# Kernel optimization log

Hardware: AMD Instinct MI355X
Metric: run time of the kernel (lower is better)

The kernel has to match this reference:

```python
import jax, jax.numpy as jnp
import numpy as np

D = 4096   # ray_hidden_dim / embed_dim
H = 2      # num_heads
E = 8192   # expert hidden dim
OUT = 1    # out_dim


def setup_inputs() -> dict:
    key = jax.random.key(0)
    ks = jax.random.split(key, 18)
    def w(k, shape, fan_in):
        return jax.random.normal(k, shape, jnp.float32) * (1.0 / np.sqrt(fan_in))
    return dict(
        ray=jax.random.uniform(ks[0], (2,), jnp.float32),
        emb1_w=w(ks[1], (D, 1), 1), emb1_b=w(ks[2], (D,), 1),
        emb2_w=w(ks[3], (D, 1), 1), emb2_b=w(ks[4], (D,), 1),
        attn_in_w=w(ks[5], (3 * D, D), D), attn_in_b=jnp.zeros((3 * D,), jnp.float32),
        attn_out_w=w(ks[6], (D, D), D), attn_out_b=jnp.zeros((D,), jnp.float32),
        ffn1_w=w(ks[7], (D, D), D), ffn1_b=w(ks[8], (D,), D),
        ffn2_w=w(ks[9], (D, D), D), ffn2_b=w(ks[10], (D,), D),
        exp_w1=w(ks[11], (E, D), D), exp_b1=w(ks[12], (E,), D),
        exp_w2=w(ks[13], (OUT, E), E), exp_b2=w(ks[14], (OUT,), E),
        idx=0,
    )


def reference(ray, emb1_w, emb1_b, emb2_w, emb2_b,
              attn_in_w, attn_in_b, attn_out_w, attn_out_b,
              ffn1_w, ffn1_b, ffn2_w, ffn2_b,
              exp_w1, exp_b1, exp_w2, exp_b2, idx):
    # per-task embeddings: Linear(1, D) + ReLU on each scalar ray component
    e1 = jax.nn.relu(ray[0:1] @ emb1_w.T + emb1_b)  # [D]
    e2 = jax.nn.relu(ray[1:2] @ emb2_w.T + emb2_b)  # [D]
    x = jnp.stack([e1, e2])                          # [L=2, D] (batch=1 squeezed)

    # multi-head self-attention (torch MHA, packed in_proj)
    qkv = x @ attn_in_w.T + attn_in_b                # [2, 3D]
    q, k, v = jnp.split(qkv, 3, axis=-1)
    hd = D // H
    q = q.reshape(2, H, hd) * jnp.float32(1.0 / np.sqrt(hd))
    k = k.reshape(2, H, hd)
    v = v.reshape(2, H, hd)
    scores = jnp.einsum('lhd,mhd->hlm', q, k)        # [H, 2, 2]
    attn = jax.nn.softmax(scores, axis=-1)
    o = jnp.einsum('hlm,mhd->lhd', attn, v).reshape(2, D)
    x = x + (o @ attn_out_w.T + attn_out_b)          # residual 1

    # FFN block with residual
    x = x + (jax.nn.relu(x @ ffn1_w.T + ffn1_b) @ ffn2_w.T + ffn2_b)

    # expert MLP (idx selects expert; n_experts=1 so idx==0) then mean over seq
    y = jax.nn.relu(x @ exp_w1.T + exp_b1) @ exp_w2.T + exp_b2  # [2, OUT]
    return jnp.mean(y, axis=0)                       # [OUT]
```

## Files before the change

kernel.cpp:

```cpp
#include <hip/hip_runtime.h>

#define D4 4096
#define E8 8192

#define OFF_X    0
#define OFF_QKV  8192
#define OFF_O    32768
#define OFF_H    40960
#define OFF_G    49152
__device__ float g_ws[65536];

__global__ void k_embed(const float* __restrict__ ray,
                        const float* __restrict__ w1,
                        const float* __restrict__ b1,
                        const float* __restrict__ w2,
                        const float* __restrict__ b2) {
    int i = blockIdx.x * blockDim.x + threadIdx.x;
    if (i < D4) {
        float r0 = ray[0], r1 = ray[1];
        g_ws[OFF_X + i]      = fmaxf(fmaf(r0, w1[i], b1[i]), 0.f);
        g_ws[OFF_X + D4 + i] = fmaxf(fmaf(r1, w2[i], b2[i]), 0.f);
    }
}

__global__ __launch_bounds__(512, 4) void k_gemv2(
        const float* __restrict__ W,
        const float* __restrict__ bias,
        int xin_off, int out_off, int resid_off,
        int R, int relu_flag) {
    __shared__ float sx[2 * D4];
    const float* xin = g_ws + xin_off;
    int tid = threadIdx.x;
    #pragma unroll
    for (int it = 0; it < (2 * D4) / (512 * 4); ++it) {
        int j = (it * 512 + tid) * 4;
        *(float4*)(sx + j) = *(const float4*)(xin + j);
    }
    __syncthreads();

    int row  = blockIdx.x * 8 + (tid >> 6);
    int lane = tid & 63;
    const float* wrow = W + (size_t)row * D4;
    float acc0 = 0.f, acc1 = 0.f;
    #pragma unroll 4
    for (int it = 0; it < D4 / (64 * 4); ++it) {
        int j = (it * 64 + lane) * 4;
        float4 wv = *(const float4*)(wrow + j);
        float4 x0 = *(const float4*)(sx + j);
        float4 x1 = *(const float4*)(sx + D4 + j);
        acc0 = fmaf(wv.x, x0.x, fmaf(wv.y, x0.y, fmaf(wv.z, x0.z, fmaf(wv.w, x0.w, acc0))));
        acc1 = fmaf(wv.x, x1.x, fmaf(wv.y, x1.y, fmaf(wv.z, x1.z, fmaf(wv.w, x1.w, acc1))));
    }
    #pragma unroll
    for (int off = 32; off; off >>= 1) {
        acc0 += __shfl_down(acc0, off);
        acc1 += __shfl_down(acc1, off);
    }
    if (lane == 0) {
        float b  = bias[row];
        float r0 = acc0 + b, r1 = acc1 + b;
        if (resid_off >= 0) {
            r0 += g_ws[resid_off + row];
            r1 += g_ws[resid_off + R + row];
        }
        if (relu_flag) { r0 = fmaxf(r0, 0.f); r1 = fmaxf(r1, 0.f); }
        g_ws[out_off + row]     = r0;
        g_ws[out_off + R + row] = r1;
    }
}

__global__ void k_attn() {
    const int HD = D4 / 2;
    const float* qkv = g_ws + OFF_QKV;
    float* o = g_ws + OFF_O;
    __shared__ float sred[8][16];
    __shared__ float sattn[2][2][2];
    int tid = threadIdx.x, lane = tid & 63, wave = tid >> 6;

    float a000 = 0.f, a001 = 0.f, a010 = 0.f, a011 = 0.f;
    float a100 = 0.f, a101 = 0.f, a110 = 0.f, a111 = 0.f;
    #pragma unroll
    for (int it = 0; it < 2; ++it) {
        int i = it * 1024 + tid;
        float q0 = qkv[0 * 3 * D4 + i];
        float q1 = qkv[1 * 3 * D4 + i];
        float k0 = qkv[0 * 3 * D4 + D4 + i];
        float k1 = qkv[1 * 3 * D4 + D4 + i];
        a000 += q0 * k0; a001 += q0 * k1;
        a010 += q1 * k0; a011 += q1 * k1;
    }
    #pragma unroll
    for (int it = 0; it < 2; ++it) {
        int i = HD + it * 1024 + tid;
        float q0 = qkv[0 * 3 * D4 + i];
        float q1 = qkv[1 * 3 * D4 + i];
        float k0 = qkv[0 * 3 * D4 + D4 + i];
        float k1 = qkv[1 * 3 * D4 + D4 + i];
        a100 += q0 * k0; a101 += q0 * k1;
        a110 += q1 * k0; a111 += q1 * k1;
    }
    #define WREDUCE(v, idx) { float t_ = (v); \
        _Pragma("unroll") \
        for (int off_ = 32; off_; off_ >>= 1) t_ += __shfl_down(t_, off_); \
        if (lane == 0) sred[idx][wave] = t_; }
    WREDUCE(a000, 0) WREDUCE(a001, 1) WREDUCE(a010, 2) WREDUCE(a011, 3)
    WREDUCE(a100, 4) WREDUCE(a101, 5) WREDUCE(a110, 6) WREDUCE(a111, 7)
    #undef WREDUCE
    __syncthreads();
    if (tid == 0) {
        float scale = rsqrtf((float)HD);
        for (int h = 0; h < 2; h++)
            for (int l = 0; l < 2; l++) {
                float s0 = 0.f, s1 = 0.f;
                for (int w = 0; w < 16; w++) {
                    s0 += sred[(h * 2 + l) * 2 + 0][w];
                    s1 += sred[(h * 2 + l) * 2 + 1][w];
                }
                s0 *= scale; s1 *= scale;
                float mx = fmaxf(s0, s1);
                float e0 = __expf(s0 - mx), e1 = __expf(s1 - mx);
                float inv = 1.f / (e0 + e1);
                sattn[h][l][0] = e0 * inv;
                sattn[h][l][1] = e1 * inv;
            }
    }
    __syncthreads();
    #pragma unroll
    for (int it = 0; it < 4; ++it) {
        int i = it * 1024 + tid;
        int h = i >> 11;
        float v0 = qkv[0 * 3 * D4 + 2 * D4 + i];
        float v1 = qkv[1 * 3 * D4 + 2 * D4 + i];
        o[i]      = sattn[h][0][0] * v0 + sattn[h][0][1] * v1;
        o[D4 + i] = sattn[h][1][0] * v0 + sattn[h][1][1] * v1;
    }
}

__global__ void k_expert_out(const float* __restrict__ w2,
                             const float* __restrict__ b2,
                             float* __restrict__ out) {
    const float* g = g_ws + OFF_G;
    __shared__ float sred[2][16];
    int tid = threadIdx.x, lane = tid & 63, wave = tid >> 6;
    float a0 = 0.f, a1 = 0.f;
    #pragma unroll
    for (int it = 0; it < E8 / 1024; ++it) {
        int e = it * 1024 + tid;
        float w = w2[e];
        a0 += w * g[e];
        a1 += w * g[E8 + e];
    }
    #pragma unroll
    for (int off = 32; off; off >>= 1) {
        a0 += __shfl_down(a0, off);
        a1 += __shfl_down(a1, off);
    }
    if (lane == 0) { sred[0][wave] = a0; sred[1][wave] = a1; }
    __syncthreads();
    if (tid == 0) {
        float b = b2[0];
        float y0 = b, y1 = b;
        for (int w = 0; w < 16; w++) { y0 += sred[0][w]; y1 += sred[1][w]; }
        out[0] = 0.5f * (y0 + y1);
    }
}

extern "C" void kernel_launch(void* const* d_in, const int* in_sizes, int n_in,
                              void* d_out, int out_size, void* d_ws, size_t ws_size,
                              hipStream_t stream) {
    const float* ray        = (const float*)d_in[0];
    const float* emb1_w     = (const float*)d_in[1];
    const float* emb1_b     = (const float*)d_in[2];
    const float* emb2_w     = (const float*)d_in[3];
    const float* emb2_b     = (const float*)d_in[4];
    const float* attn_in_w  = (const float*)d_in[5];
    const float* attn_in_b  = (const float*)d_in[6];
    const float* attn_out_w = (const float*)d_in[7];
    const float* attn_out_b = (const float*)d_in[8];
    const float* ffn1_w     = (const float*)d_in[9];
    const float* ffn1_b     = (const float*)d_in[10];
    const float* ffn2_w     = (const float*)d_in[11];
    const float* ffn2_b     = (const float*)d_in[12];
    const float* exp_w1     = (const float*)d_in[13];
    const float* exp_b1     = (const float*)d_in[14];
    const float* exp_w2     = (const float*)d_in[15];
    const float* exp_b2     = (const float*)d_in[16];
    float* out = (float*)d_out;
    (void)d_ws; (void)ws_size; (void)in_sizes; (void)n_in;

    k_embed<<<(D4 + 255) / 256, 256, 0, stream>>>(ray, emb1_w, emb1_b, emb2_w, emb2_b);
    k_gemv2<<<3 * D4 / 8, 512, 0, stream>>>(attn_in_w, attn_in_b, OFF_X, OFF_QKV, -1, 3 * D4, 0);
    k_attn<<<1, 1024, 0, stream>>>();
    k_gemv2<<<D4 / 8, 512, 0, stream>>>(attn_out_w, attn_out_b, OFF_O, OFF_X, OFF_X, D4, 0);
    k_gemv2<<<D4 / 8, 512, 0, stream>>>(ffn1_w, ffn1_b, OFF_X, OFF_H, -1, D4, 1);
    k_gemv2<<<D4 / 8, 512, 0, stream>>>(ffn2_w, ffn2_b, OFF_H, OFF_X, OFF_X, D4, 0);
    k_gemv2<<<E8 / 8, 512, 0, stream>>>(exp_w1, exp_b1, OFF_X, OFF_G, -1, E8, 1);
    k_expert_out<<<1, 1024, 0, stream>>>(exp_w2, exp_b2, out);
}
```

Before: 509.1 us.

## Restructure GEMV to one float4 per thread with two rows per block

Replaces the shared-memory-staged GEMV, where each wave loops over a full row, with a kernel that assigns two rows to a 1024-thread block. Each thread loads a single float4 from each row and reads the activation vector directly from global memory, then reduces across waves via shared memory. The aim is to raise memory-level parallelism and remove the per-block staging of x. The trade-off is many more small blocks plus an extra block-level sync and reduction per pair of rows.

```diff
diff --git a/kernel.cpp b/kernel.cpp
--- a/kernel.cpp
+++ b/kernel.cpp
@@ -23,49 +23,65 @@
     }
 }
 
-__global__ __launch_bounds__(512, 4) void k_gemv2(
+__global__ __launch_bounds__(1024) void k_gemv_row(
         const float* __restrict__ W,
         const float* __restrict__ bias,
         int xin_off, int out_off, int resid_off,
         int R, int relu_flag) {
-    __shared__ float sx[2 * D4];
+    int tid  = threadIdx.x;
+    int r0   = blockIdx.x * 2;
+    int j    = tid * 4;
     const float* xin = g_ws + xin_off;
-    int tid = threadIdx.x;
-    #pragma unroll
-    for (int it = 0; it < (2 * D4) / (512 * 4); ++it) {
-        int j = (it * 512 + tid) * 4;
-        *(float4*)(sx + j) = *(const float4*)(xin + j);
-    }
-    __syncthreads();
-
-    int row  = blockIdx.x * 8 + (tid >> 6);
-    int lane = tid & 63;
-    const float* wrow = W + (size_t)row * D4;
-    float acc0 = 0.f, acc1 = 0.f;
-    #pragma unroll 4
-    for (int it = 0; it < D4 / (64 * 4); ++it) {
-        int j = (it * 64 + lane) * 4;
-        float4 wv = *(const float4*)(wrow + j);
-        float4 x0 = *(const float4*)(sx + j);
-        float4 x1 = *(const float4*)(sx + D4 + j);
-        acc0 = fmaf(wv.x, x0.x, fmaf(wv.y, x0.y, fmaf(wv.z, x0.z, fmaf(wv.w, x0.w, acc0))));
-        acc1 = fmaf(wv.x, x1.x, fmaf(wv.y, x1.y, fmaf(wv.z, x1.z, fmaf(wv.w, x1.w, acc1))));
-    }
+    const float* w0p = W + (size_t)r0 * D4 + j;
+
+    float4 w0 = *(const float4*)(w0p);
+    float4 w1 = *(const float4*)(w0p + D4);
+    float4 x0 = *(const float4*)(xin + j);
+    float4 x1 = *(const float4*)(xin + D4 + j);
+
+    float a00 = w0.x*x0.x + w0.y*x0.y + w0.z*x0.z + w0.w*x0.w;
+    float a01 = w0.x*x1.x + w0.y*x1.y + w0.z*x1.z + w0.w*x1.w;
+    float a10 = w1.x*x0.x + w1.y*x0.y + w1.z*x0.z + w1.w*x0.w;
+    float a11 = w1.x*x1.x + w1.y*x1.y + w1.z*x1.z + w1.w*x1.w;
+
     #pragma unroll
     for (int off = 32; off; off >>= 1) {
-        acc0 += __shfl_down(acc0, off);
-        acc1 += __shfl_down(acc1, off);
-    }
+        a00 += __shfl_down(a00, off);
+        a01 += __shfl_down(a01, off);
+        a10 += __shfl_down(a10, off);
+        a11 += __shfl_down(a11, off);
+    }
+    __shared__ float sred[16][4];
+    int lane = tid & 63, wave = tid >> 6;
     if (lane == 0) {
-        float b  = bias[row];
-        float r0 = acc0 + b, r1 = acc1 + b;
+        sred[wave][0] = a00; sred[wave][1] = a01;
+        sred[wave][2] = a10; sred[wave][3] = a11;
+    }
+    __syncthreads();
+    if (tid == 0) {
+        float s00 = 0.f, s01 = 0.f, s10 = 0.f, s11 = 0.f;
+        #pragma unroll
+        for (int w = 0; w < 16; ++w) {
+            s00 += sred[w][0]; s01 += sred[w][1];
+            s10 += sred[w][2]; s11 += sred[w][3];
+        }
+        int r1i = r0 + 1;
+        float b0 = bias[r0], b1 = bias[r1i];
+        s00 += b0; s01 += b0; s10 += b1; s11 += b1;
         if (resid_off >= 0) {
-            r0 += g_ws[resid_off + row];
-            r1 += g_ws[resid_off + R + row];
+            s00 += g_ws[resid_off + r0];
+            s01 += g_ws[resid_off + R + r0];
+            s10 += g_ws[resid_off + r1i];
+            s11 += g_ws[resid_off + R + r1i];
         }
-        if (relu_flag) { r0 = fmaxf(r0, 0.f); r1 = fmaxf(r1, 0.f); }
-        g_ws[out_off + row]     = r0;
-        g_ws[out_off + R + row] = r1;
+        if (relu_flag) {
+            s00 = fmaxf(s00, 0.f); s01 = fmaxf(s01, 0.f);
+            s10 = fmaxf(s10, 0.f); s11 = fmaxf(s11, 0.f);
+        }
+        g_ws[out_off + r0]       = s00;
+        g_ws[out_off + R + r0]   = s01;
+        g_ws[out_off + r1i]      = s10;
+        g_ws[out_off + R + r1i]  = s11;
     }
 }
 
@@ -189,11 +205,11 @@
     (void)d_ws; (void)ws_size; (void)in_sizes; (void)n_in;
 
     k_embed<<<(D4 + 255) / 256, 256, 0, stream>>>(ray, emb1_w, emb1_b, emb2_w, emb2_b);
-    k_gemv2<<<3 * D4 / 8, 512, 0, stream>>>(attn_in_w, attn_in_b, OFF_X, OFF_QKV, -1, 3 * D4, 0);
+    k_gemv_row<<<3 * D4 / 2, 1024, 0, stream>>>(attn_in_w, attn_in_b, OFF_X, OFF_QKV, -1, 3 * D4, 0);
     k_attn<<<1, 1024, 0, stream>>>();
-    k_gemv2<<<D4 / 8, 512, 0, stream>>>(attn_out_w, attn_out_b, OFF_O, OFF_X, OFF_X, D4, 0);
-    k_gemv2<<<D4 / 8, 512, 0, stream>>>(ffn1_w, ffn1_b, OFF_X, OFF_H, -1, D4, 1);
-    k_gemv2<<<D4 / 8, 512, 0, stream>>>(ffn2_w, ffn2_b, OFF_H, OFF_X, OFF_X, D4, 0);
-    k_gemv2<<<E8 / 8, 512, 0, stream>>>(exp_w1, exp_b1, OFF_X, OFF_G, -1, E8, 1);
+    k_gemv_row<<<D4 / 2, 1024, 0, stream>>>(attn_out_w, attn_out_b, OFF_O, OFF_X, OFF_X, D4, 0);
+    k_gemv_row<<<D4 / 2, 1024, 0, stream>>>(ffn1_w, ffn1_b, OFF_X, OFF_H, -1, D4, 1);
+    k_gemv_row<<<D4 / 2, 1024, 0, stream>>>(ffn2_w, ffn2_b, OFF_H, OFF_X, OFF_X, D4, 0);
+    k_gemv_row<<<E8 / 2, 1024, 0, stream>>>(exp_w1, exp_b1, OFF_X, OFF_G, -1, E8, 1);
     k_expert_out<<<1, 1024, 0, stream>>>(exp_w2, exp_b2, out);
 }
```

New measurement: 512.6 us. About the same (+0.7%).

## Fuse whole forward pass into one persistent cooperative kernel with grid syncs

Applied to the files above, without the earlier changes.

Replaces eight separate launches (embed, five GEMVs, attention, expert output) with a single cooperative kernel of 256 blocks by 1024 threads that runs every stage and separates them with grid.sync. Embeddings are computed straight into shared memory, and the attention mix writes its output into shared memory so the next GEMV reads it without a global round trip. The GEMV loop now loads eight float4 weight values per batch before doing the math, to keep more memory requests in flight. The aim is to remove launch gaps and inter-kernel drain. In exchange, each block of 16 waves shares one block's resources and relies on grid-wide barriers, and the attention-score stage keeps only 8 blocks busy while the rest wait.

```diff
diff --git a/kernel.cpp b/kernel.cpp
--- a/kernel.cpp
+++ b/kernel.cpp
@@ -1,199 +1,209 @@
 #include <hip/hip_runtime.h>
+#include <hip/hip_cooperative_groups.h>
+
+namespace cg = cooperative_groups;
 
 #define D4 4096
 #define E8 8192
+#define NBLK 256
+#define NTHR 1024
+#define NWAVES (NBLK * (NTHR / 64))
 
 #define OFF_X    0
 #define OFF_QKV  8192
-#define OFF_O    32768
+#define OFF_XO   32768
 #define OFF_H    40960
-#define OFF_G    49152
-__device__ float g_ws[65536];
-
-__global__ void k_embed(const float* __restrict__ ray,
-                        const float* __restrict__ w1,
-                        const float* __restrict__ b1,
-                        const float* __restrict__ w2,
-                        const float* __restrict__ b2) {
-    int i = blockIdx.x * blockDim.x + threadIdx.x;
-    if (i < D4) {
-        float r0 = ray[0], r1 = ray[1];
-        g_ws[OFF_X + i]      = fmaxf(fmaf(r0, w1[i], b1[i]), 0.f);
-        g_ws[OFF_X + D4 + i] = fmaxf(fmaf(r1, w2[i], b2[i]), 0.f);
+#define OFF_X2   49152
+#define OFF_G    57344
+#define OFF_S    73728
+__device__ float g_ws[73744];
+
+struct P {
+    const float *ray, *e1w, *e1b, *e2w, *e2b;
+    const float *aiw, *aib, *aow, *aob;
+    const float *f1w, *f1b, *f2w, *f2b;
+    const float *xw1, *xb1, *xw2, *xb2;
+    float *out;
+};
+
+__device__ __forceinline__ void gemv2_lds(
+        const float* __restrict__ W, const float* __restrict__ bias,
+        const float* sx, float* out, const float* resid,
+        int R, int relu, int lane, int gwave)
+{
+    for (int r = gwave; r < R; r += NWAVES) {
+        const float* wrow = W + (size_t)r * D4;
+        float a0 = 0.f, a1 = 0.f;
+        #pragma unroll
+        for (int c = 0; c < 2; ++c) {
+            float4 wv[8];
+            #pragma unroll
+            for (int k = 0; k < 8; ++k)
+                wv[k] = *(const float4*)(wrow + ((c * 8 + k) * 64 + lane) * 4);
+            #pragma unroll
+            for (int k = 0; k < 8; ++k) {
+                int j = ((c * 8 + k) * 64 + lane) * 4;
+                float4 x0 = *(const float4*)(sx + j);
+                float4 x1 = *(const float4*)(sx + D4 + j);
+                a0 += wv[k].x*x0.x + wv[k].y*x0.y + wv[k].z*x0.z + wv[k].w*x0.w;
+                a1 += wv[k].x*x1.x + wv[k].y*x1.y + wv[k].z*x1.z + wv[k].w*x1.w;
+            }
+        }
+        #pragma unroll
+        for (int off = 32; off; off >>= 1) {
+            a0 += __shfl_down(a0, off);
+            a1 += __shfl_down(a1, off);
+        }
+        if (lane == 0) {
+            float b = bias[r];
+            float r0 = a0 + b, r1 = a1 + b;
+            if (resid) { r0 += resid[r]; r1 += resid[R + r]; }
+            if (relu)  { r0 = fmaxf(r0, 0.f); r1 = fmaxf(r1, 0.f); }
+            out[r] = r0; out[R + r] = r1;
+        }
     }
 }
 
-__global__ __launch_bounds__(512, 4) void k_gemv2(
-        const float* __restrict__ W,
-        const float* __restrict__ bias,
-        int xin_off, int out_off, int resid_off,
-        int R, int relu_flag) {
+__global__ __launch_bounds__(NTHR) void k_fused(P p) {
+    cg::grid_group grid = cg::this_grid();
     __shared__ float sx[2 * D4];
-    const float* xin = g_ws + xin_off;
-    int tid = threadIdx.x;
-    #pragma unroll
-    for (int it = 0; it < (2 * D4) / (512 * 4); ++it) {
-        int j = (it * 512 + tid) * 4;
-        *(float4*)(sx + j) = *(const float4*)(xin + j);
-    }
-    __syncthreads();
-
-    int row  = blockIdx.x * 8 + (tid >> 6);
-    int lane = tid & 63;
-    const float* wrow = W + (size_t)row * D4;
-    float acc0 = 0.f, acc1 = 0.f;
-    #pragma unroll 4
-    for (int it = 0; it < D4 / (64 * 4); ++it) {
-        int j = (it * 64 + lane) * 4;
-        float4 wv = *(const float4*)(wrow + j);
-        float4 x0 = *(const float4*)(sx + j);
-        float4 x1 = *(const float4*)(sx + D4 + j);
-        acc0 = fmaf(wv.x, x0.x, fmaf(wv.y, x0.y, fmaf(wv.z, x0.z, fmaf(wv.w, x0.w, acc0))));
-        acc1 = fmaf(wv.x, x1.x, fmaf(wv.y, x1.y, fmaf(wv.z, x1.z, fmaf(wv.w, x1.w, acc1))));
-    }
-    #pragma unroll
-    for (int off = 32; off; off >>= 1) {
-        acc0 += __shfl_down(acc0, off);
-        acc1 += __shfl_down(acc1, off);
-    }
-    if (lane == 0) {
-        float b  = bias[row];
-        float r0 = acc0 + b, r1 = acc1 + b;
-        if (resid_off >= 0) {
-            r0 += g_ws[resid_off + row];
-            r1 += g_ws[resid_off + R + row];
-        }
-        if (relu_flag) { r0 = fmaxf(r0, 0.f); r1 = fmaxf(r1, 0.f); }
-        g_ws[out_off + row]     = r0;
-        g_ws[out_off + R + row] = r1;
-    }
-}
-
-__global__ void k_attn() {
-    const int HD = D4 / 2;
-    const float* qkv = g_ws + OFF_QKV;
-    float* o = g_ws + OFF_O;
-    __shared__ float sred[8][16];
-    __shared__ float sattn[2][2][2];
+    __shared__ float sred[16];
+    __shared__ float sred2[16][2];
     int tid = threadIdx.x, lane = tid & 63, wave = tid >> 6;
-
-    float a000 = 0.f, a001 = 0.f, a010 = 0.f, a011 = 0.f;
-    float a100 = 0.f, a101 = 0.f, a110 = 0.f, a111 = 0.f;
-    #pragma unroll
-    for (int it = 0; it < 2; ++it) {
-        int i = it * 1024 + tid;
-        float q0 = qkv[0 * 3 * D4 + i];
-        float q1 = qkv[1 * 3 * D4 + i];
-        float k0 = qkv[0 * 3 * D4 + D4 + i];
-        float k1 = qkv[1 * 3 * D4 + D4 + i];
-        a000 += q0 * k0; a001 += q0 * k1;
-        a010 += q1 * k0; a011 += q1 * k1;
-    }
-    #pragma unroll
-    for (int it = 0; it < 2; ++it) {
-        int i = HD + it * 1024 + tid;
-        float q0 = qkv[0 * 3 * D4 + i];
-        float q1 = qkv[1 * 3 * D4 + i];
-        float k0 = qkv[0 * 3 * D4 + D4 + i];
-        float k1 = qkv[1 * 3 * D4 + D4 + i];
-        a100 += q0 * k0; a101 += q0 * k1;
-        a110 += q1 * k0; a111 += q1 * k1;
-    }
-    #define WREDUCE(v, idx) { float t_ = (v); \
-        _Pragma("unroll") \
-        for (int off_ = 32; off_; off_ >>= 1) t_ += __shfl_down(t_, off_); \
-        if (lane == 0) sred[idx][wave] = t_; }
-    WREDUCE(a000, 0) WREDUCE(a001, 1) WREDUCE(a010, 2) WREDUCE(a011, 3)
-    WREDUCE(a100, 4) WREDUCE(a101, 5) WREDUCE(a110, 6) WREDUCE(a111, 7)
-    #undef WREDUCE
-    __syncthreads();
-    if (tid == 0) {
-        float scale = rsqrtf((float)HD);
-        for (int h = 0; h < 2; h++)
-            for (int l = 0; l < 2; l++) {
-                float s0 = 0.f, s1 = 0.f;
-                for (int w = 0; w < 16; w++) {
-                    s0 += sred[(h * 2 + l) * 2 + 0][w];
-                    s1 += sred[(h * 2 + l) * 2 + 1][w];
-                }
-                s0 *= scale; s1 *= scale;
+    int gwave = blockIdx.x * (NTHR / 64) + wave;
+
+    float r0 = p.ray[0], r1 = p.ray[1];
+    #pragma unroll
+    for (int it = 0; it < 4; ++it) {
+        int i = it * NTHR + tid;
+        sx[i]      = fmaxf(fmaf(r0, p.e1w[i], p.e1b[i]), 0.f);
+        sx[D4 + i] = fmaxf(fmaf(r1, p.e2w[i], p.e2b[i]), 0.f);
+    }
+    __syncthreads();
+    if (blockIdx.x == 0) {
+        #pragma unroll
+        for (int it = 0; it < 8; ++it) {
+            int i = it * NTHR + tid;
+            g_ws[OFF_X + i] = sx[i];
+        }
+    }
+    gemv2_lds(p.aiw, p.aib, sx, g_ws + OFF_QKV, nullptr, 3 * D4, 0, lane, gwave);
+    grid.sync();
+
+    if (blockIdx.x < 8) {
+        int b = blockIdx.x;
+        int h = b >> 2, l = (b >> 1) & 1, m = b & 1;
+        const float* q = g_ws + OFF_QKV + l * 3 * D4 + h * 2048;
+        const float* k = g_ws + OFF_QKV + m * 3 * D4 + D4 + h * 2048;
+        float acc = q[tid * 2] * k[tid * 2] + q[tid * 2 + 1] * k[tid * 2 + 1];
+        #pragma unroll
+        for (int off = 32; off; off >>= 1) acc += __shfl_down(acc, off);
+        if (lane == 0) sred[wave] = acc;
+        __syncthreads();
+        if (tid == 0) {
+            float s = 0.f;
+            for (int w = 0; w < 16; ++w) s += sred[w];
+            g_ws[OFF_S + b] = s;
+        }
+    }
+    grid.sync();
+
+    {
+        float scale = rsqrtf(2048.f);
+        float pr[2][2][2];
+        #pragma unroll
+        for (int h = 0; h < 2; ++h)
+            #pragma unroll
+            for (int l = 0; l < 2; ++l) {
+                float s0 = g_ws[OFF_S + h * 4 + l * 2 + 0] * scale;
+                float s1 = g_ws[OFF_S + h * 4 + l * 2 + 1] * scale;
                 float mx = fmaxf(s0, s1);
                 float e0 = __expf(s0 - mx), e1 = __expf(s1 - mx);
                 float inv = 1.f / (e0 + e1);
-                sattn[h][l][0] = e0 * inv;
-                sattn[h][l][1] = e1 * inv;
+                pr[h][l][0] = e0 * inv; pr[h][l][1] = e1 * inv;
             }
-    }
-    __syncthreads();
-    #pragma unroll
-    for (int it = 0; it < 4; ++it) {
-        int i = it * 1024 + tid;
-        int h = i >> 11;
-        float v0 = qkv[0 * 3 * D4 + 2 * D4 + i];
-        float v1 = qkv[1 * 3 * D4 + 2 * D4 + i];
-        o[i]      = sattn[h][0][0] * v0 + sattn[h][0][1] * v1;
-        o[D4 + i] = sattn[h][1][0] * v0 + sattn[h][1][1] * v1;
-    }
-}
-
-__global__ void k_expert_out(const float* __restrict__ w2,
-                             const float* __restrict__ b2,
-                             float* __restrict__ out) {
-    const float* g = g_ws + OFF_G;
-    __shared__ float sred[2][16];
-    int tid = threadIdx.x, lane = tid & 63, wave = tid >> 6;
-    float a0 = 0.f, a1 = 0.f;
-    #pragma unroll
-    for (int it = 0; it < E8 / 1024; ++it) {
-        int e = it * 1024 + tid;
-        float w = w2[e];
-        a0 += w * g[e];
-        a1 += w * g[E8 + e];
-    }
-    #pragma unroll
-    for (int off = 32; off; off >>= 1) {
-        a0 += __shfl_down(a0, off);
-        a1 += __shfl_down(a1, off);
-    }
-    if (lane == 0) { sred[0][wave] = a0; sred[1][wave] = a1; }
-    __syncthreads();
-    if (tid == 0) {
-        float b = b2[0];
-        float y0 = b, y1 = b;
-        for (int w = 0; w < 16; w++) { y0 += sred[0][w]; y1 += sred[1][w]; }
-        out[0] = 0.5f * (y0 + y1);
+        #pragma unroll
+        for (int it = 0; it < 4; ++it) {
+            int i = it * NTHR + tid;
+            const int h = it >> 1;
+            float v0 = g_ws[OFF_QKV + 0 * 3 * D4 + 2 * D4 + i];
+            float v1 = g_ws[OFF_QKV + 1 * 3 * D4 + 2 * D4 + i];
+            sx[i]      = pr[h][0][0] * v0 + pr[h][0][1] * v1;
+            sx[D4 + i] = pr[h][1][0] * v0 + pr[h][1][1] * v1;
+        }
+        __syncthreads();
+        gemv2_lds(p.aow, p.aob, sx, g_ws + OFF_XO, g_ws + OFF_X, D4, 0, lane, gwave);
+    }
+    grid.sync();
+
+    #pragma unroll
+    for (int it = 0; it < 2; ++it) {
+        int j = (it * NTHR + tid) * 4;
+        *(float4*)(sx + j) = *(const float4*)(g_ws + OFF_XO + j);
+    }
+    __syncthreads();
+    gemv2_lds(p.f1w, p.f1b, sx, g_ws + OFF_H, nullptr, D4, 1, lane, gwave);
+    grid.sync();
+
+    #pragma unroll
+    for (int it = 0; it < 2; ++it) {
+        int j = (it * NTHR + tid) * 4;
+        *(float4*)(sx + j) = *(const float4*)(g_ws + OFF_H + j);
+    }
+    __syncthreads();
+    gemv2_lds(p.f2w, p.f2b, sx, g_ws + OFF_X2, g_ws + OFF_XO, D4, 0, lane, gwave);
+    grid.sync();
+
+    #pragma unroll
+    for (int it = 0; it < 2; ++it) {
+        int j = (it * NTHR + tid) * 4;
+        *(float4*)(sx + j) = *(const float4*)(g_ws + OFF_X2 + j);
+    }
+    __syncthreads();
+    gemv2_lds(p.xw1, p.xb1, sx, g_ws + OFF_G, nullptr, E8, 1, lane, gwave);
+    grid.sync();
+
+    if (blockIdx.x == 0) {
+        float a0 = 0.f, a1 = 0.f;
+        #pragma unroll
+        for (int it = 0; it < 8; ++it) {
+            int e = it * NTHR + tid;
+            float w = p.xw2[e];
+            a0 += w * g_ws[OFF_G + e];
+            a1 += w * g_ws[OFF_G + E8 + e];
+        }
+        #pragma unroll
+        for (int off = 32; off; off >>= 1) {
+            a0 += __shfl_down(a0, off);
+            a1 += __shfl_down(a1, off);
+        }
+        if (lane == 0) { sred2[wave][0] = a0; sred2[wave][1] = a1; }
+        __syncthreads();
+        if (tid == 0) {
+            float y0 = 0.f, y1 = 0.f;
+            for (int w = 0; w < 16; ++w) { y0 += sred2[w][0]; y1 += sred2[w][1]; }
+            p.out[0] = 0.5f * (y0 + y1) + p.xb2[0];
+        }
     }
 }
 
 extern "C" void kernel_launch(void* const* d_in, const int* in_sizes, int n_in,
                               void* d_out, int out_size, void* d_ws, size_t ws_size,
                               hipStream_t stream) {
-    const float* ray        = (const float*)d_in[0];
-    const float* emb1_w     = (const float*)d_in[1];
-    const float* emb1_b     = (const float*)d_in[2];
-    const float* emb2_w     = (const float*)d_in[3];
-    const float* emb2_b     = (const float*)d_in[4];
-    const float* attn_in_w  = (const float*)d_in[5];
-    const float* attn_in_b  = (const float*)d_in[6];
-    const float* attn_out_w = (const float*)d_in[7];
-    const float* attn_out_b = (const float*)d_in[8];
-    const float* ffn1_w     = (const float*)d_in[9];
-    const float* ffn1_b     = (const float*)d_in[10];
-    const float* ffn2_w     = (const float*)d_in[11];
-    const float* ffn2_b     = (const float*)d_in[12];
-    const float* exp_w1     = (const float*)d_in[13];
-    const float* exp_b1     = (const float*)d_in[14];
-    const float* exp_w2     = (const float*)d_in[15];
-    const float* exp_b2     = (const float*)d_in[16];
-    float* out = (float*)d_out;
     (void)d_ws; (void)ws_size; (void)in_sizes; (void)n_in;
-
-    k_embed<<<(D4 + 255) / 256, 256, 0, stream>>>(ray, emb1_w, emb1_b, emb2_w, emb2_b);
-    k_gemv2<<<3 * D4 / 8, 512, 0, stream>>>(attn_in_w, attn_in_b, OFF_X, OFF_QKV, -1, 3 * D4, 0);
-    k_attn<<<1, 1024, 0, stream>>>();
-    k_gemv2<<<D4 / 8, 512, 0, stream>>>(attn_out_w, attn_out_b, OFF_O, OFF_X, OFF_X, D4, 0);
-    k_gemv2<<<D4 / 8, 512, 0, stream>>>(ffn1_w, ffn1_b, OFF_X, OFF_H, -1, D4, 1);
-    k_gemv2<<<D4 / 8, 512, 0, stream>>>(ffn2_w, ffn2_b, OFF_H, OFF_X, OFF_X, D4, 0);
-    k_gemv2<<<E8 / 8, 512, 0, stream>>>(exp_w1, exp_b1, OFF_X, OFF_G, -1, E8, 1);
-    k_expert_out<<<1, 1024, 0, stream>>>(exp_w2, exp_b2, out);
+    P p;
+    p.ray = (const float*)d_in[0];
+    p.e1w = (const float*)d_in[1];  p.e1b = (const float*)d_in[2];
+    p.e2w = (const float*)d_in[3];  p.e2b = (const float*)d_in[4];
+    p.aiw = (const float*)d_in[5];  p.aib = (const float*)d_in[6];
+    p.aow = (const float*)d_in[7];  p.aob = (const float*)d_in[8];
+    p.f1w = (const float*)d_in[9];  p.f1b = (const float*)d_in[10];
+    p.f2w = (const float*)d_in[11]; p.f2b = (const float*)d_in[12];
+    p.xw1 = (const float*)d_in[13]; p.xb1 = (const float*)d_in[14];
+    p.xw2 = (const float*)d_in[15]; p.xb2 = (const float*)d_in[16];
+    p.out = (float*)d_out;
+
+    void* args[] = { &p };
+    hipLaunchCooperativeKernel((void*)k_fused, dim3(NBLK), dim3(NTHR),
+                               args, 0u, stream);
 }
```

Result: slower. 846.3 us (+66.2%).

## Split GEMV rows across two waves and preload weights into registers

Applied to the files above, without the earlier changes.

Replaces the LDS-staged GEMV with a kernel where each pair of waves covers one weight row, each wave taking half of it. All eight float4 weight loads are issued up front into registers, and the activations are read straight from global memory instead of being copied into LDS. The two half-row results are combined through a small shared buffer. The aim is more loads in flight and no 32KB LDS fill plus barrier per block, so the weight stream runs closer to memory bandwidth. The cost is more blocks, a cross-wave reduction, and activation re-reads that depend on L2 hits.

```diff
diff --git a/kernel.cpp b/kernel.cpp
--- a/kernel.cpp
+++ b/kernel.cpp
@@ -23,49 +23,46 @@
     }
 }
 
-__global__ __launch_bounds__(512, 4) void k_gemv2(
+__global__ __launch_bounds__(256, 8) void k_gemv_h(
         const float* __restrict__ W,
         const float* __restrict__ bias,
         int xin_off, int out_off, int resid_off,
         int R, int relu_flag) {
-    __shared__ float sx[2 * D4];
-    const float* xin = g_ws + xin_off;
-    int tid = threadIdx.x;
+    int tid = threadIdx.x, lane = tid & 63, wave = tid >> 6;
+    int r  = blockIdx.x * 2 + (wave >> 1);
+    int hf = wave & 1;
+    const float* wp = W + (size_t)r * D4 + hf * 2048;
+    const float* xp = g_ws + xin_off + hf * 2048;
+
+    float4 wv[8];
     #pragma unroll
-    for (int it = 0; it < (2 * D4) / (512 * 4); ++it) {
-        int j = (it * 512 + tid) * 4;
-        *(float4*)(sx + j) = *(const float4*)(xin + j);
-    }
-    __syncthreads();
+    for (int k = 0; k < 8; ++k)
+        wv[k] = *(const float4*)(wp + (k * 64 + lane) * 4);
 
-    int row  = blockIdx.x * 8 + (tid >> 6);
-    int lane = tid & 63;
-    const float* wrow = W + (size_t)row * D4;
-    float acc0 = 0.f, acc1 = 0.f;
-    #pragma unroll 4
-    for (int it = 0; it < D4 / (64 * 4); ++it) {
-        int j = (it * 64 + lane) * 4;
-        float4 wv = *(const float4*)(wrow + j);
-        float4 x0 = *(const float4*)(sx + j);
-        float4 x1 = *(const float4*)(sx + D4 + j);
-        acc0 = fmaf(wv.x, x0.x, fmaf(wv.y, x0.y, fmaf(wv.z, x0.z, fmaf(wv.w, x0.w, acc0))));
-        acc1 = fmaf(wv.x, x1.x, fmaf(wv.y, x1.y, fmaf(wv.z, x1.z, fmaf(wv.w, x1.w, acc1))));
+    float a0 = 0.f, a1 = 0.f;
+    #pragma unroll
+    for (int k = 0; k < 8; ++k) {
+        int j = (k * 64 + lane) * 4;
+        float4 x0 = *(const float4*)(xp + j);
+        float4 x1 = *(const float4*)(xp + D4 + j);
+        a0 += wv[k].x*x0.x + wv[k].y*x0.y + wv[k].z*x0.z + wv[k].w*x0.w;
+        a1 += wv[k].x*x1.x + wv[k].y*x1.y + wv[k].z*x1.z + wv[k].w*x1.w;
     }
     #pragma unroll
     for (int off = 32; off; off >>= 1) {
-        acc0 += __shfl_down(acc0, off);
-        acc1 += __shfl_down(acc1, off);
+        a0 += __shfl_down(a0, off);
+        a1 += __shfl_down(a1, off);
     }
-    if (lane == 0) {
-        float b  = bias[row];
-        float r0 = acc0 + b, r1 = acc1 + b;
-        if (resid_off >= 0) {
-            r0 += g_ws[resid_off + row];
-            r1 += g_ws[resid_off + R + row];
-        }
-        if (relu_flag) { r0 = fmaxf(r0, 0.f); r1 = fmaxf(r1, 0.f); }
-        g_ws[out_off + row]     = r0;
-        g_ws[out_off + R + row] = r1;
+    __shared__ float sred[4][2];
+    if (lane == 0) { sred[wave][0] = a0; sred[wave][1] = a1; }
+    __syncthreads();
+    if (tid < 4) {
+        int rl = tid >> 1, tok = tid & 1;
+        int rr = blockIdx.x * 2 + rl;
+        float s = sred[rl * 2][tok] + sred[rl * 2 + 1][tok] + bias[rr];
+        if (resid_off >= 0) s += g_ws[resid_off + tok * R + rr];
+        if (relu_flag) s = fmaxf(s, 0.f);
+        g_ws[out_off + tok * R + rr] = s;
     }
 }
 
@@ -189,11 +186,11 @@
     (void)d_ws; (void)ws_size; (void)in_sizes; (void)n_in;
 
     k_embed<<<(D4 + 255) / 256, 256, 0, stream>>>(ray, emb1_w, emb1_b, emb2_w, emb2_b);
-    k_gemv2<<<3 * D4 / 8, 512, 0, stream>>>(attn_in_w, attn_in_b, OFF_X, OFF_QKV, -1, 3 * D4, 0);
+    k_gemv_h<<<3 * D4 / 2, 256, 0, stream>>>(attn_in_w, attn_in_b, OFF_X, OFF_QKV, -1, 3 * D4, 0);
     k_attn<<<1, 1024, 0, stream>>>();
-    k_gemv2<<<D4 / 8, 512, 0, stream>>>(attn_out_w, attn_out_b, OFF_O, OFF_X, OFF_X, D4, 0);
-    k_gemv2<<<D4 / 8, 512, 0, stream>>>(ffn1_w, ffn1_b, OFF_X, OFF_H, -1, D4, 1);
-    k_gemv2<<<D4 / 8, 512, 0, stream>>>(ffn2_w, ffn2_b, OFF_H, OFF_X, OFF_X, D4, 0);
-    k_gemv2<<<E8 / 8, 512, 0, stream>>>(exp_w1, exp_b1, OFF_X, OFF_G, -1, E8, 1);
+    k_gemv_h<<<D4 / 2, 256, 0, stream>>>(attn_out_w, attn_out_b, OFF_O, OFF_X, OFF_X, D4, 0);
+    k_gemv_h<<<D4 / 2, 256, 0, stream>>>(ffn1_w, ffn1_b, OFF_X, OFF_H, -1, D4, 1);
+    k_gemv_h<<<D4 / 2, 256, 0, stream>>>(ffn2_w, ffn2_b, OFF_H, OFF_X, OFF_X, D4, 0);
+    k_gemv_h<<<E8 / 2, 256, 0, stream>>>(exp_w1, exp_b1, OFF_X, OFF_G, -1, E8, 1);
     k_expert_out<<<1, 1024, 0, stream>>>(exp_w2, exp_b2, out);
 }
```

After: 513.6 us. About the same (+0.9%).
